# Optimization experiments

Measured on AMD Instinct MI355X. Metric: run time of the kernel, lower is better.

## Reference

```python
import jax, jax.numpy as jnp
import numpy as np

IN_CH = 512
OUT_CH = 3
W_DIM = 512
CLAMP = 256.0

# setup_filter([1,3,3,1]): outer product, normalized to sum 1 (separable FIR)
_f1 = np.array([1.0, 3.0, 3.0, 1.0], dtype=np.float32)
_f2 = np.outer(_f1, _f1)
_f2 = _f2 / _f2.sum()
FIR = jnp.asarray(_f2)  # [4,4], symmetric so flipping is a no-op


def setup_inputs() -> dict:
    key = jax.random.key(0)
    ks = jax.random.split(key, 5)
    return {
        "x": jax.random.normal(ks[0], (8, IN_CH, 128, 128), jnp.float32),
        "w": jax.random.normal(ks[1], (8, W_DIM), jnp.float32),
        "skip": jax.random.normal(ks[2], (8, OUT_CH, 64, 64), jnp.float32),
        "affine_w": jax.random.normal(ks[3], (IN_CH, W_DIM), jnp.float32),
        "affine_b": jnp.ones((IN_CH,), jnp.float32),  # bias_init=1
        "weight": jax.random.normal(ks[4], (OUT_CH, IN_CH, 1, 1), jnp.float32),
        "bias": jnp.zeros((OUT_CH,), jnp.float32),
    }


def _upsample2d(s):
    # upfirdn2d.upsample2d(up=2): zero-insert, pad, FIR filter, gain = up**2 = 4.
    # lax lhs_dilation=2 gives 2H-1 samples (no trailing zero); torch ref pads
    # (2,1) on the 2H-length sequence -> equivalent lax padding is (2,2).
    C = s.shape[1]
    k = jnp.tile((FIR * 4.0)[None, None], (C, 1, 1, 1))  # [C,1,4,4] depthwise
    return jax.lax.conv_general_dilated(
        s, k, window_strides=(1, 1), padding=((2, 2), (2, 2)),
        lhs_dilation=(2, 2),
        dimension_numbers=("NCHW", "OIHW", "NCHW"),
        feature_group_count=C,
    )


def reference(x, w, skip, affine_w, affine_b, weight, bias):
    # affine DenseLayer: default activation='lrelu' (alpha=0.2, gain=sqrt(2))
    affine_gain = 1.0 / np.sqrt(W_DIM)
    styles = jax.nn.leaky_relu(w @ (affine_w * affine_gain).T + affine_b, 0.2)
    styles = styles * np.float32(np.sqrt(2.0))  # [B, IN_CH]

    # modulated 1x1 conv, demodulate=False, groups=batch ->
    # out[b,o,h,w] = sum_i (weight[o,i]*wg) * styles[b,i] * x[b,i,h,w]
    wm = weight[:, :, 0, 0] * (1.0 / IN_CH)  # weight_gain = 1/in_channels
    y = jnp.einsum("oi,bi,bihw->bohw", wm, styles, x)

    # bias_act: linear act + clamp
    y = jnp.clip(y + bias[None, :, None, None], -CLAMP, CLAMP)

    return y + _upsample2d(skip)
```

## Files before the change

### kernel.cpp

```cpp
#include <hip/hip_runtime.h>
#include <math.h>


#define IN_CH 512
#define OUT_CH 3
#define NPIX 16384
#define NB 8

__global__ __launch_bounds__(256) void coeff_kernel(
    const float* __restrict__ w, const float* __restrict__ aw,
    const float* __restrict__ ab, const float* __restrict__ wt,
    float* __restrict__ coeff) {
  const int b  = blockIdx.x >> 6;
  const int rg = blockIdx.x & 63;
  const int tid = threadIdx.x;
  __shared__ float wv[512];
  wv[tid]       = w[b * 512 + tid];
  wv[tid + 256] = w[b * 512 + 256 + tid];
  __syncthreads();
  const int wave = tid >> 6, lane = tid & 63;
  const float gain = 1.0f / sqrtf(512.0f);
  #pragma unroll
  for (int r = 0; r < 2; ++r) {
    const int i = rg * 8 + wave * 2 + r;
    const float* row = aw + (size_t)i * 512;
    float s = 0.f;
    #pragma unroll
    for (int k = 0; k < 8; ++k) s += row[lane + 64 * k] * wv[lane + 64 * k];
    #pragma unroll
    for (int off = 32; off >= 1; off >>= 1) s += __shfl_xor(s, off, 64);
    if (lane == 0) {
      float v = s * gain + ab[i];
      v = (v > 0.f ? v : 0.2f * v) * 1.41421356237f;
      #pragma unroll
      for (int o = 0; o < OUT_CH; ++o)
        coeff[b * (OUT_CH * IN_CH) + o * IN_CH + i] =
            wt[o * IN_CH + i] * (1.0f / 512.0f) * v;
    }
  }
}

__global__ __launch_bounds__(256) void main_kernel(
    const float* __restrict__ x, const float* __restrict__ coeff,
    const float* __restrict__ bias, const float* __restrict__ skip,
    float* __restrict__ out) {
  const int b   = blockIdx.x >> 8;
  const int g   = blockIdx.x & 255;
  const int p0  = g * 64;
  const int tid = threadIdx.x;
  const int col   = tid & 15;
  const int split = tid >> 4;

  __shared__ float lds_c[16 * 32 * 4];
  for (int idx = tid; idx < 2048; idx += 256) {
    const int s = idx >> 7, rem = idx & 127, k = rem >> 2, o = rem & 3;
    lds_c[idx] = (o < 3)
        ? coeff[b * (OUT_CH * IN_CH) + o * IN_CH + s * 32 + k]
        : 0.f;
  }

  float up = 0.f;
  if (tid < 192) {
    const int o = tid >> 6;
    const int l = tid & 63;
    const int p = p0 + l;
    const int yy = p >> 7, xx = p & 127;
    int iy0, ix0; float wy0, wy1, wx0, wx1;
    if (yy & 1) { iy0 = (yy - 1) >> 1; wy0 = 3.f; wy1 = 1.f; }
    else        { iy0 = (yy >> 1) - 1; wy0 = 1.f; wy1 = 3.f; }
    if (xx & 1) { ix0 = (xx - 1) >> 1; wx0 = 3.f; wx1 = 1.f; }
    else        { ix0 = (xx >> 1) - 1; wx0 = 1.f; wx1 = 3.f; }
    const float* sp = skip + ((size_t)(b * OUT_CH + o)) * 4096;
    float s00 = (iy0 >= 0     && ix0 >= 0    ) ? sp[iy0 * 64 + ix0]           : 0.f;
    float s01 = (iy0 >= 0     && ix0 + 1 < 64) ? sp[iy0 * 64 + ix0 + 1]       : 0.f;
    float s10 = (iy0 + 1 < 64 && ix0 >= 0    ) ? sp[(iy0 + 1) * 64 + ix0]     : 0.f;
    float s11 = (iy0 + 1 < 64 && ix0 + 1 < 64) ? sp[(iy0 + 1) * 64 + ix0 + 1] : 0.f;
    up = (wy0 * (wx0 * s00 + wx1 * s01) + wy1 * (wx0 * s10 + wx1 * s11)) * (1.f / 16.f);
  }

  __syncthreads();

  const float* xp = x + ((size_t)(b * IN_CH + split * 32)) * NPIX + p0 + col * 4;
  const float* cp = lds_c + split * 128;

  float acc[12];
  #pragma unroll
  for (int j = 0; j < 12; ++j) acc[j] = 0.f;

  #pragma unroll 8
  for (int k = 0; k < 32; ++k) {
    float4 xv = *reinterpret_cast<const float4*>(xp + (size_t)k * NPIX);
    float4 c4 = *reinterpret_cast<const float4*>(cp + k * 4);
    acc[0] += c4.x * xv.x; acc[1]  += c4.x * xv.y; acc[2]  += c4.x * xv.z; acc[3]  += c4.x * xv.w;
    acc[4] += c4.y * xv.x; acc[5]  += c4.y * xv.y; acc[6]  += c4.y * xv.z; acc[7]  += c4.y * xv.w;
    acc[8] += c4.z * xv.x; acc[9]  += c4.z * xv.y; acc[10] += c4.z * xv.z; acc[11] += c4.z * xv.w;
  }

  #pragma unroll
  for (int j = 0; j < 12; ++j) {
    acc[j] += __shfl_xor(acc[j], 16, 64);
    acc[j] += __shfl_xor(acc[j], 32, 64);
  }
  __shared__ float red[4][16][13];
  const int wave = tid >> 6, lane = tid & 63;
  if (lane < 16) {
    #pragma unroll
    for (int j = 0; j < 12; ++j) red[wave][lane][j] = acc[j];
  }
  __syncthreads();

  if (tid < 192) {
    const int o = tid >> 6;
    const int l = tid & 63;
    const int c = l >> 2, j = o * 4 + (l & 3);
    float v = red[0][c][j] + red[1][c][j] + red[2][c][j] + red[3][c][j] + bias[o];
    v = fminf(fmaxf(v, -256.f), 256.f);
    out[((size_t)(b * OUT_CH + o)) * NPIX + p0 + l] = v + up;
  }
}

extern "C" void kernel_launch(void* const* d_in, const int* in_sizes, int n_in,
                              void* d_out, int out_size, void* d_ws, size_t ws_size,
                              hipStream_t stream) {
  const float* x        = (const float*)d_in[0];
  const float* w        = (const float*)d_in[1];
  const float* skip     = (const float*)d_in[2];
  const float* affine_w = (const float*)d_in[3];
  const float* affine_b = (const float*)d_in[4];
  const float* weight   = (const float*)d_in[5];
  const float* bias     = (const float*)d_in[6];
  float* out   = (float*)d_out;
  float* coeff = (float*)d_ws;

  coeff_kernel<<<512, 256, 0, stream>>>(w, affine_w, affine_b, weight, coeff);
  main_kernel<<<NB * 256, 256, 0, stream>>>(x, coeff, bias, skip, out);
}
```

Baseline: 53.61 us.

## Widen main kernel pixel tile to 256 and split channels across four waves

Each block now covers 256 pixels instead of 64. The 512 input channels are split into four 128-channel slices, one per wave, so each wave streams a full 1 KB contiguous row per channel, and the cross-lane shuffle reduction is replaced by a plain LDS reduction. Grid size falls from 2048 to 512 blocks, and each thread does 128 sequential loads instead of 32. This cuts per-block overhead such as the coeff LDS fill, but gives fewer blocks to hide the latency of a memory-bound x stream on a large GPU.

```diff
diff --git a/kernel.cpp b/kernel.cpp
--- a/kernel.cpp
+++ b/kernel.cpp
@@ -44,51 +44,56 @@
     const float* __restrict__ x, const float* __restrict__ coeff,
     const float* __restrict__ bias, const float* __restrict__ skip,
     float* __restrict__ out) {
-  const int b   = blockIdx.x >> 8;
-  const int g   = blockIdx.x & 255;
-  const int p0  = g * 64;
+  const int b   = blockIdx.x >> 6;
+  const int g   = blockIdx.x & 63;
+  const int p0  = g * 256;
   const int tid = threadIdx.x;
-  const int col   = tid & 15;
-  const int split = tid >> 4;
+  const int col   = tid & 63;
+  const int split = tid >> 6;
 
-  __shared__ float lds_c[16 * 32 * 4];
+  __shared__ float lds_c[4 * 128 * 4];
   for (int idx = tid; idx < 2048; idx += 256) {
-    const int s = idx >> 7, rem = idx & 127, k = rem >> 2, o = rem & 3;
+    const int s = idx >> 9, rem = idx & 511, k = rem >> 2, o = rem & 3;
     lds_c[idx] = (o < 3)
-        ? coeff[b * (OUT_CH * IN_CH) + o * IN_CH + s * 32 + k]
+        ? coeff[b * (OUT_CH * IN_CH) + o * IN_CH + s * 128 + k]
         : 0.f;
   }
 
-  float up = 0.f;
-  if (tid < 192) {
-    const int o = tid >> 6;
-    const int l = tid & 63;
-    const int p = p0 + l;
+  float up[3];
+  {
+    const int p = p0 + tid;
     const int yy = p >> 7, xx = p & 127;
     int iy0, ix0; float wy0, wy1, wx0, wx1;
     if (yy & 1) { iy0 = (yy - 1) >> 1; wy0 = 3.f; wy1 = 1.f; }
     else        { iy0 = (yy >> 1) - 1; wy0 = 1.f; wy1 = 3.f; }
     if (xx & 1) { ix0 = (xx - 1) >> 1; wx0 = 3.f; wx1 = 1.f; }
     else        { ix0 = (xx >> 1) - 1; wx0 = 1.f; wx1 = 3.f; }
-    const float* sp = skip + ((size_t)(b * OUT_CH + o)) * 4096;
-    float s00 = (iy0 >= 0     && ix0 >= 0    ) ? sp[iy0 * 64 + ix0]           : 0.f;
-    float s01 = (iy0 >= 0     && ix0 + 1 < 64) ? sp[iy0 * 64 + ix0 + 1]       : 0.f;
-    float s10 = (iy0 + 1 < 64 && ix0 >= 0    ) ? sp[(iy0 + 1) * 64 + ix0]     : 0.f;
-    float s11 = (iy0 + 1 < 64 && ix0 + 1 < 64) ? sp[(iy0 + 1) * 64 + ix0 + 1] : 0.f;
-    up = (wy0 * (wx0 * s00 + wx1 * s01) + wy1 * (wx0 * s10 + wx1 * s11)) * (1.f / 16.f);
+    const float wyx00 = wy0 * wx0 * (1.f / 16.f), wyx01 = wy0 * wx1 * (1.f / 16.f);
+    const float wyx10 = wy1 * wx0 * (1.f / 16.f), wyx11 = wy1 * wx1 * (1.f / 16.f);
+    const bool y0ok = (iy0 >= 0), y1ok = (iy0 + 1 < 64);
+    const bool x0ok = (ix0 >= 0), x1ok = (ix0 + 1 < 64);
+    #pragma unroll
+    for (int o = 0; o < OUT_CH; ++o) {
+      const float* sp = skip + ((size_t)(b * OUT_CH + o)) * 4096;
+      float s00 = (y0ok && x0ok) ? sp[iy0 * 64 + ix0]           : 0.f;
+      float s01 = (y0ok && x1ok) ? sp[iy0 * 64 + ix0 + 1]       : 0.f;
+      float s10 = (y1ok && x0ok) ? sp[(iy0 + 1) * 64 + ix0]     : 0.f;
+      float s11 = (y1ok && x1ok) ? sp[(iy0 + 1) * 64 + ix0 + 1] : 0.f;
+      up[o] = wyx00 * s00 + wyx01 * s01 + wyx10 * s10 + wyx11 * s11;
+    }
   }
 
   __syncthreads();
 
-  const float* xp = x + ((size_t)(b * IN_CH + split * 32)) * NPIX + p0 + col * 4;
-  const float* cp = lds_c + split * 128;
+  const float* xp = x + ((size_t)(b * IN_CH + split * 128)) * NPIX + p0 + col * 4;
+  const float* cp = lds_c + split * 512;
 
   float acc[12];
   #pragma unroll
   for (int j = 0; j < 12; ++j) acc[j] = 0.f;
 
-  #pragma unroll 8
-  for (int k = 0; k < 32; ++k) {
+  #pragma unroll 16
+  for (int k = 0; k < 128; ++k) {
     float4 xv = *reinterpret_cast<const float4*>(xp + (size_t)k * NPIX);
     float4 c4 = *reinterpret_cast<const float4*>(cp + k * 4);
     acc[0] += c4.x * xv.x; acc[1]  += c4.x * xv.y; acc[2]  += c4.x * xv.z; acc[3]  += c4.x * xv.w;
@@ -96,26 +101,20 @@
     acc[8] += c4.z * xv.x; acc[9]  += c4.z * xv.y; acc[10] += c4.z * xv.z; acc[11] += c4.z * xv.w;
   }
 
+  __shared__ float red[4][64][13];
   #pragma unroll
-  for (int j = 0; j < 12; ++j) {
-    acc[j] += __shfl_xor(acc[j], 16, 64);
-    acc[j] += __shfl_xor(acc[j], 32, 64);
-  }
-  __shared__ float red[4][16][13];
-  const int wave = tid >> 6, lane = tid & 63;
-  if (lane < 16) {
-    #pragma unroll
-    for (int j = 0; j < 12; ++j) red[wave][lane][j] = acc[j];
-  }
+  for (int j = 0; j < 12; ++j) red[split][col][j] = acc[j];
   __syncthreads();
 
-  if (tid < 192) {
-    const int o = tid >> 6;
-    const int l = tid & 63;
-    const int c = l >> 2, j = o * 4 + (l & 3);
-    float v = red[0][c][j] + red[1][c][j] + red[2][c][j] + red[3][c][j] + bias[o];
-    v = fminf(fmaxf(v, -256.f), 256.f);
-    out[((size_t)(b * OUT_CH + o)) * NPIX + p0 + l] = v + up;
+  {
+    const int c = tid >> 2, s = tid & 3;
+    #pragma unroll
+    for (int o = 0; o < OUT_CH; ++o) {
+      const int j = o * 4 + s;
+      float v = red[0][c][j] + red[1][c][j] + red[2][c][j] + red[3][c][j] + bias[o];
+      v = fminf(fmaxf(v, -256.f), 256.f);
+      out[((size_t)(b * OUT_CH + o)) * NPIX + p0 + tid] = v + up[o];
+    }
   }
 }
 
@@ -133,5 +132,5 @@
   float* coeff = (float*)d_ws;
 
   coeff_kernel<<<512, 256, 0, stream>>>(w, affine_w, affine_b, weight, coeff);
-  main_kernel<<<NB * 256, 256, 0, stream>>>(x, coeff, bias, skip, out);
+  main_kernel<<<NB * 64, 256, 0, stream>>>(x, coeff, bias, skip, out);
 }
```

Result: slower. 56.87 us (+6.1%).
